# Kernel optimization log

Measured on AMD Instinct MI355X. Metric: run time of the kernel, lower is better.

## Reference

```python
import jax, jax.numpy as jnp
import numpy as np
from jax import lax

B, T, V, E, H = 32, 512, 32000, 300, 256
TRANSITION = 0.1
TEMP = 0.01
BUDGET_PCT = 30.0
NEG = -1e9


def setup_inputs() -> dict:
    key = jax.random.key(0)
    ks = jax.random.split(key, 10)
    sc = lambda k, shape, s=0.05: (jax.random.normal(k, shape, jnp.float32) * s)
    x = jax.random.randint(ks[0], (B, T), 0, V)
    mask = jnp.ones((B, T), bool)
    embed = sc(ks[1], (V, E), 0.1)
    w_ih_f = sc(ks[2], (E, 4 * H))
    w_hh_f = sc(ks[3], (H, 4 * H))
    b_f = jnp.zeros((4 * H,), jnp.float32)
    w_ih_b = sc(ks[4], (E, 4 * H))
    w_hh_b = sc(ks[5], (H, 4 * H))
    b_b = jnp.zeros((4 * H,), jnp.float32)
    w_out = sc(ks[6], (2 * H, 1), 0.1)
    b_out = jnp.zeros((1,), jnp.float32)
    return {"x": x, "current_epoch": 0, "mask": mask, "embed": embed,
            "w_ih_f": w_ih_f, "w_hh_f": w_hh_f, "b_f": b_f,
            "w_ih_b": w_ih_b, "w_hh_b": w_hh_b, "b_b": b_b,
            "w_out": w_out, "b_out": b_out}


def _lstm_dir(emb, mask, Wi, Wh, b):
    # masked LSTM equivalent to pack_padded_sequence; gate order i,f,g,o (torch)
    bs, tl, _ = emb.shape
    h0 = jnp.zeros((bs, Wh.shape[0]), emb.dtype)
    xg = emb @ Wi + b  # [B,T,4H]

    def step(carry, inp):
        h, c = carry
        xg_t, m_t = inp
        g = xg_t + h @ Wh
        i, f, gg, o = jnp.split(g, 4, axis=-1)
        i = jax.nn.sigmoid(i); f = jax.nn.sigmoid(f)
        gg = jnp.tanh(gg); o = jax.nn.sigmoid(o)
        c_new = f * c + i * gg
        h_new = o * jnp.tanh(c_new)
        m = m_t[:, None]
        h_new = jnp.where(m, h_new, h)
        c_new = jnp.where(m, c_new, c)
        return (h_new, c_new), jnp.where(m, h_new, 0.0)

    _, hs = lax.scan(step, (h0, h0), (xg.transpose(1, 0, 2), mask.T))
    return hs.transpose(1, 0, 2)


def _forward(x, mask, embed, w_ih_f, w_hh_f, b_f, w_ih_b, w_hh_b, b_b, w_out, b_out):
    emb = embed[x]  # [B,T,E] (dropout disabled / eval)
    h_f = _lstm_dir(emb, mask, w_ih_f, w_hh_f, b_f)
    h_b = jnp.flip(_lstm_dir(jnp.flip(emb, 1), jnp.flip(mask, 1), w_ih_b, w_hh_b, b_b), 1)
    h = jnp.concatenate([h_f, h_b], axis=-1)  # [B,T,2H]
    scores = (h @ w_out + b_out)[..., 0]  # [B,T]

    lengths = mask.sum(1)
    pos = jnp.arange(T)
    # unary for state 0 (selected); padded positions forced off
    u0 = jnp.where(pos[None, :] < lengths[:, None], scores / TEMP, NEG)
    # transition[t,0,0] = transition/temp for t <= length, else 0;  t in 0..T
    tvals = jnp.where(jnp.arange(T + 1)[None, :] <= lengths[:, None], TRANSITION / TEMP, 0.0)
    budget = jnp.round(BUDGET_PCT / 100.0 * lengths)
    Cmax = int(round(BUDGET_PCT / 100.0 * T)) + 1  # static count dim

    def logZ(u0_):
        alpha = jnp.full((u0_.shape[0], Cmax, 2), NEG, u0_.dtype)
        alpha = alpha.at[:, 1, 0].set(u0_[:, 0] + tvals[:, 0])  # start in state0 (count 1)
        alpha = alpha.at[:, 0, 1].set(0.0)                       # start in state1 (count 0)

        def step(a, inp):
            u0_t, t_t = inp
            a_shift = jnp.concatenate([jnp.full((a.shape[0], 1, 2), NEG, a.dtype), a[:, :-1, :]], axis=1)
            m0 = jnp.logaddexp(a_shift[..., 0] + t_t[:, None], a_shift[..., 1])
            m1 = jnp.logaddexp(a[..., 0], a[..., 1])
            return jnp.stack([u0_t[:, None] + m0, m1], axis=-1), None

        alpha, _ = lax.scan(step, alpha, (u0_[:, 1:].T, tvals[:, 1:T].T))
        final = jnp.stack([alpha[..., 0] + tvals[:, T][:, None], alpha[..., 1]], axis=-1)
        allowed = (jnp.arange(Cmax)[None, :] <= budget[:, None])[..., None]
        lz = jax.nn.logsumexp(jnp.where(allowed, final, NEG).reshape(final.shape[0], -1), axis=-1)
        return lz.sum()

    # marginal p(z_i=1) = d logZ / d u0_i  (budget-constrained chain marginals)
    z = jax.grad(logZ)(u0)
    return jnp.where(mask, z, 0.0)


def reference(x, current_epoch, mask, embed, w_ih_f, w_hh_f, b_f, w_ih_b, w_hh_b, b_b, w_out, b_out):
    return _forward(x, mask, embed, w_ih_f, w_hh_f, b_f, w_ih_b, w_hh_b, b_b, w_out, b_out)
```

## Files before the change

kernel.cpp:

```cpp
#include <hip/hip_runtime.h>
#include <math.h>

#define BB 32
#define TT_LEN 512
#define EE 300
#define HH 256
#define G4 1024
#define CMAX 155
#define TRANS_T 10.0f
#define NEGF -1.0e9f
#define INV_TEMP 100.0f
#define AST_STRIDE 159

#define NCH_L2 8
#define NREG 24

typedef _Float16 half2v __attribute__((ext_vector_type(2)));
typedef _Float16 half8 __attribute__((ext_vector_type(8)));
typedef float f32x4 __attribute__((ext_vector_type(4)));

__device__ __forceinline__ float la(float x, float y) {
  float m = fmaxf(x, y);
  float d = fminf(x, y) - m;
  return m + __logf(1.0f + __expf(d));
}

__device__ __forceinline__ float sigm(float x) {
  return 1.0f / (1.0f + __expf(-x));
}

__device__ __forceinline__ float dot2acc(unsigned int wd, unsigned int hd, float acc) {
#if __has_builtin(__builtin_amdgcn_fdot2)
  return __builtin_amdgcn_fdot2(__builtin_bit_cast(half2v, wd),
                                __builtin_bit_cast(half2v, hd), acc, false);
#else
  half2v a = __builtin_bit_cast(half2v, wd);
  half2v b = __builtin_bit_cast(half2v, hd);
  return acc + (float)a.x * (float)b.x + (float)a.y * (float)b.y;
#endif
}

__device__ __forceinline__ unsigned int packh(float a, float b) {
  half2v hp;
  hp.x = (_Float16)a;
  hp.y = (_Float16)b;
  return __builtin_bit_cast(unsigned int, hp);
}

__global__ void prep_weights(const float* wi_f, const float* wi_b,
                             const float* wh_f, const float* wh_b,
                             const float* b_f, const float* b_b,
                             unsigned int* wi_frag, float* b_p,
                             unsigned int* wlds_h, unsigned int* wstr_h) {
  int idx = blockIdx.x * blockDim.x + threadIdx.x;
  int stride = gridDim.x * blockDim.x;
  for (int i = idx; i < 2 * 64 * 10 * 64 * 4; i += stride) {
    int u4 = i >> 2, d = i & 3;
    int lane = u4 & 63;
    int kk = (u4 >> 6) % 10;
    int nb = (u4 / 640) & 63;
    int dir = u4 / (640 * 64);
    int l15 = lane & 15, quad = lane >> 4;
    int n = nb * 16 + l15;
    int g = n & 3, u = n >> 2;
    int k0 = kk * 32 + quad * 8 + 2 * d;
    const float* src = dir ? wi_b : wi_f;
    float v0 = (k0 < EE) ? src[(size_t)k0 * G4 + g * HH + u] : 0.0f;
    float v1 = (k0 + 1 < EE) ? src[(size_t)(k0 + 1) * G4 + g * HH + u] : 0.0f;
    wi_frag[i] = packh(v0, v1);
  }
  for (int i = idx; i < 2 * NCH_L2 * 4096; i += stride) {
    int dir = i / (NCH_L2 * 4096);
    int r = i % (NCH_L2 * 4096);
    int c = r / 4096;
    int r2 = r % 4096;
    int j = r2 >> 2, d = r2 & 3;
    int g = j & 3, u = j >> 2;
    int k0 = 8 * c + 2 * d;
    const float* src = dir ? wh_b : wh_f;
    wlds_h[i] = packh(src[k0 * G4 + g * HH + u], src[(k0 + 1) * G4 + g * HH + u]);
  }
  for (int i = idx; i < 2 * NREG * 4096; i += stride) {
    int dir = i / (NREG * 4096);
    int r = i % (NREG * 4096);
    int gch = r / 4096;
    int r2 = r % 4096;
    int j = r2 >> 2, d = r2 & 3;
    int g = j & 3, u = j >> 2;
    int k0 = 64 + 8 * gch + 2 * d;
    const float* src = dir ? wh_b : wh_f;
    wstr_h[i] = packh(src[k0 * G4 + g * HH + u], src[(k0 + 1) * G4 + g * HH + u]);
  }
  for (int i = idx; i < 2 * G4; i += stride) {
    int dir = i / G4;
    int j = i % G4;
    int g = j & 3, u = j >> 2;
    const float* src = dir ? b_b : b_f;
    b_p[i] = src[g * HH + u];
  }
}

__global__ void gather_emb(const int* x, const float* embed, uint4* emb_frag) {
  int mblk = blockIdx.x;
  int t = threadIdx.x;
  __shared__ int xs[16];
  if (t < 16) xs[t] = x[mblk * 16 + t];
  __syncthreads();
  for (int slot = t; slot < 640; slot += 256) {
    int kk = slot >> 6;
    int lane = slot & 63;
    int l15 = lane & 15, quad = lane >> 4;
    int row = xs[l15];
    int kbase = kk * 32 + quad * 8;
    const float* src = embed + (size_t)row * EE;
    float v[8];
#pragma unroll
    for (int e = 0; e < 8; ++e) v[e] = (kbase + e < EE) ? src[kbase + e] : 0.0f;
    uint4 o;
    o.x = packh(v[0], v[1]);
    o.y = packh(v[2], v[3]);
    o.z = packh(v[4], v[5]);
    o.w = packh(v[6], v[7]);
    emb_frag[(size_t)(mblk * 10 + kk) * 64 + lane] = o;
  }
}

__global__ __launch_bounds__(256) void xg_mfma(
    const uint4* __restrict__ emb_frag, const uint4* __restrict__ wi_frag,
    const float* __restrict__ b_p, float* __restrict__ xg) {
  int dir = blockIdx.z;
  int w = threadIdx.x >> 6;
  int lane = threadIdx.x & 63;
  int l15 = lane & 15, quad = lane >> 4;
  int mblk = blockIdx.y * 4 + w;

  const uint4* abase = emb_frag + (size_t)mblk * 10 * 64 + lane;
  f32x4 acc[4];
#pragma unroll
  for (int nt = 0; nt < 4; ++nt) acc[nt] = (f32x4){0.f, 0.f, 0.f, 0.f};

#pragma unroll
  for (int kk = 0; kk < 10; ++kk) {
    half8 a = __builtin_bit_cast(half8, abase[kk * 64]);
#pragma unroll
    for (int nt = 0; nt < 4; ++nt) {
      int nb = blockIdx.x * 4 + nt;
      half8 b = __builtin_bit_cast(
          half8, wi_frag[((size_t)(dir * 64 + nb) * 10 + kk) * 64 + lane]);
      acc[nt] = __builtin_amdgcn_mfma_f32_16x16x32_f16(a, b, acc[nt], 0, 0, 0);
    }
  }
#pragma unroll
  for (int nt = 0; nt < 4; ++nt) {
    int n = (blockIdx.x * 4 + nt) * 16 + l15;
    float bias = b_p[dir * G4 + n];
#pragma unroll
    for (int r = 0; r < 4; ++r) {
      int m = mblk * 16 + quad * 4 + r;
      xg[((size_t)dir * (BB * TT_LEN) + m) * G4 + n] = acc[nt][r] + bias;
    }
  }
}

__global__ __launch_bounds__(512, 2) void lstm_ck(
    const float* __restrict__ xg, const unsigned int* __restrict__ wlds_h,
    const uint4* __restrict__ wstr, const float* __restrict__ w_out,
    float* __restrict__ scores_part) {
  int bid = blockIdx.x;
  int dir = bid >> 5, b = bid & 31;
  int t = threadIdx.x;
  int lane = t & 63, wid = t >> 6;

  __shared__ uint4 wlds[NCH_L2 * 1024];
  __shared__ uint4 hpk4[32];
  __shared__ float gates[1024];
  __shared__ float wpart[2][4];

  const uint4* wsrcl = (const uint4*)wlds_h + (size_t)dir * (NCH_L2 * 1024);
  for (int i = t; i < NCH_L2 * 1024; i += 512) wlds[i] = wsrcl[i];
  const uint4* wsb = wstr + (size_t)dir * (NREG * 1024);
  uint4 wr0[NREG], wr1[NREG];
#pragma unroll
  for (int g = 0; g < NREG; ++g) {
    wr0[g] = wsb[g * 1024 + t];
    wr1[g] = wsb[g * 1024 + t + 512];
  }
  if (t < 32) hpk4[t] = uint4{0, 0, 0, 0};
  __syncthreads();

  const float* xgbase =
      xg + (size_t)(dir * (BB * TT_LEN) + b * TT_LEN) * G4 + t;
  float wo = (t < HH) ? w_out[dir * HH + t] : 0.0f;
  float cstate = 0.0f;

  int t0 = dir ? (TT_LEN - 1) : 0;
  float xgn0 = xgbase[(size_t)t0 * G4];
  float xgn1 = xgbase[(size_t)t0 * G4 + 512];

#pragma unroll 1
  for (int s = 0; s < TT_LEN; ++s) {
    int tt = dir ? (TT_LEN - 1 - s) : s;
    float acc0a = xgn0, acc1a = xgn1;
    float acc0b = 0.0f, acc1b = 0.0f;
    if (s + 1 < TT_LEN) {
      int t2 = dir ? (TT_LEN - 2 - s) : (s + 1);
      xgn0 = xgbase[(size_t)t2 * G4];
      xgn1 = xgbase[(size_t)t2 * G4 + 512];
    }
#pragma unroll
    for (int c = 0; c < NCH_L2; ++c) {
      uint4 h = hpk4[c];
      uint4 w0 = wlds[c * 1024 + t];
      uint4 w1 = wlds[c * 1024 + 512 + t];
      acc0a = dot2acc(w0.x, h.x, acc0a);
      acc0a = dot2acc(w0.y, h.y, acc0a);
      acc0a = dot2acc(w0.z, h.z, acc0a);
      acc0a = dot2acc(w0.w, h.w, acc0a);
      acc1a = dot2acc(w1.x, h.x, acc1a);
      acc1a = dot2acc(w1.y, h.y, acc1a);
      acc1a = dot2acc(w1.z, h.z, acc1a);
      acc1a = dot2acc(w1.w, h.w, acc1a);
    }
#pragma unroll
    for (int g = 0; g < NREG; ++g) {
      uint4 h = hpk4[NCH_L2 + g];
      if (g < 12) {
        acc0a = dot2acc(wr0[g].x, h.x, acc0a);
        acc0a = dot2acc(wr0[g].y, h.y, acc0a);
        acc0a = dot2acc(wr0[g].z, h.z, acc0a);
        acc0a = dot2acc(wr0[g].w, h.w, acc0a);
        acc1a = dot2acc(wr1[g].x, h.x, acc1a);
        acc1a = dot2acc(wr1[g].y, h.y, acc1a);
        acc1a = dot2acc(wr1[g].z, h.z, acc1a);
        acc1a = dot2acc(wr1[g].w, h.w, acc1a);
      } else {
        acc0b = dot2acc(wr0[g].x, h.x, acc0b);
        acc0b = dot2acc(wr0[g].y, h.y, acc0b);
        acc0b = dot2acc(wr0[g].z, h.z, acc0b);
        acc0b = dot2acc(wr0[g].w, h.w, acc0b);
        acc1b = dot2acc(wr1[g].x, h.x, acc1b);
        acc1b = dot2acc(wr1[g].y, h.y, acc1b);
        acc1b = dot2acc(wr1[g].z, h.z, acc1b);
        acc1b = dot2acc(wr1[g].w, h.w, acc1b);
      }
    }
    gates[t] = acc0a + acc0b;
    gates[512 + t] = acc1a + acc1b;
    __syncthreads();

    if (t < HH) {
      float4 g4 = ((const float4*)gates)[t];
      float ig = sigm(g4.x);
      float fg = sigm(g4.y);
      float gg = tanhf(g4.z);
      float og = sigm(g4.w);
      cstate = fg * cstate + ig * gg;
      float h = og * tanhf(cstate);
      float prod = h * wo;
#pragma unroll
      for (int off = 32; off > 0; off >>= 1) prod += __shfl_down(prod, off, 64);
      if (lane == 0) wpart[s & 1][wid] = prod;
      float hn = __shfl_down(h, 1, 64);
      if (!(t & 1)) ((unsigned int*)hpk4)[t >> 1] = packh(h, hn);
    }
    __syncthreads();
    if (t == 0) {
      scores_part[(size_t)(dir * BB + b) * TT_LEN + tt] =
          wpart[s & 1][0] + wpart[s & 1][1] + wpart[s & 1][2] + wpart[s & 1][3];
    }
  }
}

__global__ __launch_bounds__(128) void dp3(const float* __restrict__ scores_part,
                                           const float* __restrict__ b_out,
                                           float* __restrict__ ast_g,
                                           float* __restrict__ bst_g,
                                           float* __restrict__ lzv) {
  int b = blockIdx.x;
  int l = threadIdx.x & 63;
  int w = threadIdx.x >> 6;
  const float* spf = scores_part + (size_t)b * TT_LEN;
  const float* spb = scores_part + (size_t)(BB + b) * TT_LEN;
  float bo = b_out[0];

  float ur[8];
#pragma unroll
  for (int i = 0; i < 8; ++i)
    ur[i] = (spf[i * 64 + l] + spb[i * 64 + l] + bo) * INV_TEMP;

  if (w == 0) {
    float* ast = ast_g + (size_t)b * TT_LEN * AST_STRIDE;
    int lm1 = (l + 63) & 63;
    float a0[3], a1[3];
    float u00 = __shfl(ur[0], 0, 64);
    a0[0] = (l == 1) ? (u00 + TRANS_T) : NEGF;
    a0[1] = NEGF;
    a0[2] = NEGF;
    a1[0] = (l == 0) ? 0.0f : NEGF;
    a1[1] = NEGF;
    a1[2] = NEGF;
    ast[l] = a0[0];
    ast[64 + l] = a0[1];
    if (l < 27) ast[128 + l] = a0[2];

#pragma unroll
    for (int ch = 0; ch < 8; ++ch) {
      float uc = ur[ch];
#pragma unroll 4
      for (int tt = (ch == 0 ? 1 : 0); tt < 64; ++tt) {
        int t = ch * 64 + tt;
        float u0t = __shfl(uc, tt, 64);
        float w0a = __shfl(a0[0], lm1, 64);
        float w1a = __shfl(a0[1], lm1, 64);
        float w2a = __shfl(a0[2], lm1, 64);
        float w0b = __shfl(a1[0], lm1, 64);
        float w1b = __shfl(a1[1], lm1, 64);
        float w2b = __shfl(a1[2], lm1, 64);
        float p0a = (l == 0) ? NEGF : w0a;
        float p1a = (l == 0) ? w0a : w1a;
        float p2a = (l == 0) ? w1a : w2a;
        float p0b = (l == 0) ? NEGF : w0b;
        float p1b = (l == 0) ? w0b : w1b;
        float p2b = (l == 0) ? w1b : w2b;
        float n00 = u0t + la(p0a + TRANS_T, p0b);
        float n01 = u0t + la(p1a + TRANS_T, p1b);
        float n02 = u0t + la(p2a + TRANS_T, p2b);
        float n10 = la(a0[0], a1[0]);
        float n11 = la(a0[1], a1[1]);
        float n12 = la(a0[2], a1[2]);
        a0[0] = n00;
        a0[1] = n01;
        a0[2] = (l < 27) ? n02 : NEGF;
        a1[0] = n10;
        a1[1] = n11;
        a1[2] = (l < 27) ? n12 : NEGF;
        float* astr = ast + (size_t)t * AST_STRIDE;
        astr[l] = a0[0];
        astr[64 + l] = a0[1];
        if (l < 27) astr[128 + l] = a0[2];
      }
    }
    float f00 = a0[0] + TRANS_T, f01 = a0[1] + TRANS_T, f02 = a0[2] + TRANS_T;
    float m = fmaxf(fmaxf(fmaxf(f00, f01), fmaxf(f02, a1[0])),
                    fmaxf(a1[1], a1[2]));
#pragma unroll
    for (int off = 32; off > 0; off >>= 1) m = fmaxf(m, __shfl_xor(m, off, 64));
    float es = __expf(f00 - m) + __expf(f01 - m) + __expf(f02 - m) +
               __expf(a1[0] - m) + __expf(a1[1] - m) + __expf(a1[2] - m);
#pragma unroll
    for (int off = 32; off > 0; off >>= 1) es += __shfl_xor(es, off, 64);
    if (l == 0) lzv[b] = m + __logf(es);
  } else {
    float* bst = bst_g + (size_t)b * TT_LEN * AST_STRIDE;
    int lp1 = (l + 1) & 63;
    float b0[3], b1[3];
    b0[0] = TRANS_T;
    b0[1] = TRANS_T;
    b0[2] = (l < 27) ? TRANS_T : NEGF;
    b1[0] = 0.0f;
    b1[1] = 0.0f;
    b1[2] = (l < 27) ? 0.0f : NEGF;
    {
      float* br = bst + (size_t)(TT_LEN - 1) * AST_STRIDE;
      br[l] = b0[0];
      br[64 + l] = b0[1];
      if (l < 27) br[128 + l] = b0[2];
    }
#pragma unroll
    for (int ch = 7; ch >= 0; --ch) {
      float uc = ur[ch];
#pragma unroll 4
      for (int tt = 63; tt >= (ch == 0 ? 1 : 0); --tt) {
        int t = ch * 64 + tt;
        float u0t = __shfl(uc, tt, 64);
        float w0 = __shfl(b0[0], lp1, 64);
        float w1 = __shfl(b0[1], lp1, 64);
        float w2 = __shfl(b0[2], lp1, 64);
        float x2 = (l == 63) ? NEGF : w2;
        float x1 = (l == 63) ? w2 : w1;
        float x0 = (l == 63) ? w1 : w0;
        float nb00 = la(u0t + TRANS_T + x0, b1[0]);
        float nb01 = la(u0t + TRANS_T + x1, b1[1]);
        float nb02 = la(u0t + TRANS_T + x2, b1[2]);
        float nb10 = la(u0t + x0, b1[0]);
        float nb11 = la(u0t + x1, b1[1]);
        float nb12 = la(u0t + x2, b1[2]);
        b0[0] = nb00;
        b0[1] = nb01;
        b0[2] = (l < 27) ? nb02 : NEGF;
        b1[0] = nb10;
        b1[1] = nb11;
        b1[2] = (l < 27) ? nb12 : NEGF;
        float* br = bst + (size_t)(t - 1) * AST_STRIDE;
        br[l] = b0[0];
        br[64 + l] = b0[1];
        if (l < 27) br[128 + l] = b0[2];
      }
    }
  }
}

__global__ __launch_bounds__(256) void marg(const float* __restrict__ ast_g,
                                            const float* __restrict__ bst_g,
                                            const float* __restrict__ lzv,
                                            float* __restrict__ out) {
  int row = blockIdx.x * 4 + (threadIdx.x >> 6);
  int l = threadIdx.x & 63;
  int b = row >> 9;
  const float* ar = ast_g + (size_t)row * AST_STRIDE;
  const float* br = bst_g + (size_t)row * AST_STRIDE;
  float lz = lzv[b];
  float s = __expf(ar[l] + br[l] - lz) + __expf(ar[64 + l] + br[64 + l] - lz) +
            ((l < 27) ? __expf(ar[128 + l] + br[128 + l] - lz) : 0.0f);
#pragma unroll
  for (int off = 32; off > 0; off >>= 1) s += __shfl_xor(s, off, 64);
  if (l == 0) out[row] = s;
}

extern "C" void kernel_launch(void* const* d_in, const int* in_sizes, int n_in,
                              void* d_out, int out_size, void* d_ws, size_t ws_size,
                              hipStream_t stream) {
  const int* x = (const int*)d_in[0];
  const float* embed = (const float*)d_in[3];
  const float* wi_f = (const float*)d_in[4];
  const float* wh_f = (const float*)d_in[5];
  const float* bf = (const float*)d_in[6];
  const float* wi_b = (const float*)d_in[7];
  const float* wh_b = (const float*)d_in[8];
  const float* bbias = (const float*)d_in[9];
  const float* w_out = (const float*)d_in[10];
  const float* b_out = (const float*)d_in[11];

  float* ws = (float*)d_ws;
  float* b_p = ws;
  unsigned int* wlds_h = (unsigned int*)(b_p + 2 * G4);
  unsigned int* wstr_h = wlds_h + 2 * NCH_L2 * 4096;
  unsigned int* wi_frag = wstr_h + 2 * NREG * 4096;
  uint4* emb_frag = (uint4*)(wi_frag + 2 * 64 * 10 * 64 * 4);
  float* bst_g = (float*)emb_frag;
  float* xg = (float*)(emb_frag + (size_t)1024 * 10 * 64);
  float* scores_part = xg + (size_t)2 * BB * TT_LEN * G4;
  float* lzv = scores_part + 2 * BB * TT_LEN;
  float* ast_g = lzv + 64;
  float* outp = (float*)d_out;

  prep_weights<<<256, 256, 0, stream>>>(wi_f, wi_b, wh_f, wh_b, bf, bbias,
                                        wi_frag, b_p, wlds_h, wstr_h);
  gather_emb<<<(BB * TT_LEN) / 16, 256, 0, stream>>>(x, embed, emb_frag);
  dim3 g1(16, 256, 2);
  xg_mfma<<<g1, 256, 0, stream>>>(emb_frag, (const uint4*)wi_frag, b_p, xg);
  lstm_ck<<<64, 512, 0, stream>>>(xg, wlds_h, (const uint4*)wstr_h, w_out,
                                  scores_part);
  dp3<<<BB, 128, 0, stream>>>(scores_part, b_out, ast_g, bst_g, lzv);
  marg<<<(BB * TT_LEN) / 4, 256, 0, stream>>>(ast_g, bst_g, lzv, outp);
}
```

Baseline: 1.553 ms.

## Batch LSTM recurrence over 16 sequences per block using MFMA

Replaces the per-sequence dot2 LSTM recurrence (64 blocks, one batch row each) with an MFMA-based recurrence where each block handles 16 batch rows of one direction. The recurrent weights are split between registers and LDS, h is kept in swizzled LDS as fp16, and xg is stored in fp16 fragment layout to halve traffic. The score projection moves to a separate kernel that reads a stored fp16 h tensor. This cuts the per-step matvec cost with matrix cores, but only 4 blocks run, and it adds fp16 rounding of xg and h plus an extra global round trip for h.

```diff
diff --git a/kernel.cpp b/kernel.cpp
--- a/kernel.cpp
+++ b/kernel.cpp
@@ -12,9 +12,6 @@
 #define INV_TEMP 100.0f
 #define AST_STRIDE 159
 
-#define NCH_L2 8
-#define NREG 24
-
 typedef _Float16 half2v __attribute__((ext_vector_type(2)));
 typedef _Float16 half8 __attribute__((ext_vector_type(8)));
 typedef float f32x4 __attribute__((ext_vector_type(4)));
@@ -29,15 +26,10 @@
   return 1.0f / (1.0f + __expf(-x));
 }
 
-__device__ __forceinline__ float dot2acc(unsigned int wd, unsigned int hd, float acc) {
-#if __has_builtin(__builtin_amdgcn_fdot2)
-  return __builtin_amdgcn_fdot2(__builtin_bit_cast(half2v, wd),
-                                __builtin_bit_cast(half2v, hd), acc, false);
-#else
-  half2v a = __builtin_bit_cast(half2v, wd);
-  half2v b = __builtin_bit_cast(half2v, hd);
-  return acc + (float)a.x * (float)b.x + (float)a.y * (float)b.y;
-#endif
+__device__ __forceinline__ float tanh_f(float x) {
+  x = fminf(fmaxf(x, -15.f), 15.f);
+  float e = __expf(2.f * x);
+  return (e - 1.f) * __frcp_rn(e + 1.f);
 }
 
 __device__ __forceinline__ unsigned int packh(float a, float b) {
@@ -47,11 +39,27 @@
   return __builtin_bit_cast(unsigned int, hp);
 }
 
+__device__ __forceinline__ float2 h2f(unsigned int d) {
+  half2v h = __builtin_bit_cast(half2v, d);
+  return make_float2((float)h.x, (float)h.y);
+}
+
+__device__ __forceinline__ unsigned short f16b(float x) {
+  _Float16 h = (_Float16)x;
+  return __builtin_bit_cast(unsigned short, h);
+}
+
+__device__ __forceinline__ int nmap_col(int n) {
+  int g = (n >> 4) & 3;
+  int u = (n >> 7) * 32 + ((n >> 6) & 1) * 16 + (n & 15);
+  return g * HH + u;
+}
+
 __global__ void prep_weights(const float* wi_f, const float* wi_b,
                              const float* wh_f, const float* wh_b,
                              const float* b_f, const float* b_b,
                              unsigned int* wi_frag, float* b_p,
-                             unsigned int* wlds_h, unsigned int* wstr_h) {
+                             uint4* whr, uint4* whl) {
   int idx = blockIdx.x * blockDim.x + threadIdx.x;
   int stride = gridDim.x * blockDim.x;
   for (int i = idx; i < 2 * 64 * 10 * 64 * 4; i += stride) {
@@ -61,50 +69,46 @@
     int nb = (u4 / 640) & 63;
     int dir = u4 / (640 * 64);
     int l15 = lane & 15, quad = lane >> 4;
-    int n = nb * 16 + l15;
-    int g = n & 3, u = n >> 2;
+    int col = nmap_col(nb * 16 + l15);
     int k0 = kk * 32 + quad * 8 + 2 * d;
     const float* src = dir ? wi_b : wi_f;
-    float v0 = (k0 < EE) ? src[(size_t)k0 * G4 + g * HH + u] : 0.0f;
-    float v1 = (k0 + 1 < EE) ? src[(size_t)(k0 + 1) * G4 + g * HH + u] : 0.0f;
+    float v0 = (k0 < EE) ? src[(size_t)k0 * G4 + col] : 0.0f;
+    float v1 = (k0 + 1 < EE) ? src[(size_t)(k0 + 1) * G4 + col] : 0.0f;
     wi_frag[i] = packh(v0, v1);
   }
-  for (int i = idx; i < 2 * NCH_L2 * 4096; i += stride) {
-    int dir = i / (NCH_L2 * 4096);
-    int r = i % (NCH_L2 * 4096);
-    int c = r / 4096;
-    int r2 = r % 4096;
-    int j = r2 >> 2, d = r2 & 3;
-    int g = j & 3, u = j >> 2;
-    int k0 = 8 * c + 2 * d;
+  for (int i = idx; i < 2 * 8 * 64 * 64; i += stride) {
+    int lane = i & 63;
+    int nb = (i >> 6) & 63;
+    int kt = (i >> 12) & 7;
+    int dir = i >> 15;
+    int c = lane & 15, q = lane >> 4;
+    int col = nmap_col(nb * 16 + c);
+    int k0 = kt * 32 + q * 8;
     const float* src = dir ? wh_b : wh_f;
-    wlds_h[i] = packh(src[k0 * G4 + g * HH + u], src[(k0 + 1) * G4 + g * HH + u]);
-  }
-  for (int i = idx; i < 2 * NREG * 4096; i += stride) {
-    int dir = i / (NREG * 4096);
-    int r = i % (NREG * 4096);
-    int gch = r / 4096;
-    int r2 = r % 4096;
-    int j = r2 >> 2, d = r2 & 3;
-    int g = j & 3, u = j >> 2;
-    int k0 = 64 + 8 * gch + 2 * d;
-    const float* src = dir ? wh_b : wh_f;
-    wstr_h[i] = packh(src[k0 * G4 + g * HH + u], src[(k0 + 1) * G4 + g * HH + u]);
+    uint4 o;
+    o.x = packh(src[(size_t)(k0 + 0) * G4 + col], src[(size_t)(k0 + 1) * G4 + col]);
+    o.y = packh(src[(size_t)(k0 + 2) * G4 + col], src[(size_t)(k0 + 3) * G4 + col]);
+    o.z = packh(src[(size_t)(k0 + 4) * G4 + col], src[(size_t)(k0 + 5) * G4 + col]);
+    o.w = packh(src[(size_t)(k0 + 6) * G4 + col], src[(size_t)(k0 + 7) * G4 + col]);
+    if (kt < 6)
+      whr[((size_t)(dir * 6 + kt) * 64 + nb) * 64 + lane] = o;
+    else
+      whl[((size_t)(dir * 2 + kt - 6) * 64 + nb) * 64 + lane] = o;
   }
   for (int i = idx; i < 2 * G4; i += stride) {
     int dir = i / G4;
     int j = i % G4;
-    int g = j & 3, u = j >> 2;
     const float* src = dir ? b_b : b_f;
-    b_p[i] = src[g * HH + u];
+    b_p[i] = src[nmap_col(j)];
   }
 }
 
 __global__ void gather_emb(const int* x, const float* embed, uint4* emb_frag) {
   int mblk = blockIdx.x;
   int t = threadIdx.x;
+  int bg = mblk >> 9, tloc = mblk & 511;
   __shared__ int xs[16];
-  if (t < 16) xs[t] = x[mblk * 16 + t];
+  if (t < 16) xs[t] = x[(bg * 16 + t) * TT_LEN + tloc];
   __syncthreads();
   for (int slot = t; slot < 640; slot += 256) {
     int kk = slot >> 6;
@@ -127,11 +131,11 @@
 
 __global__ __launch_bounds__(256) void xg_mfma(
     const uint4* __restrict__ emb_frag, const uint4* __restrict__ wi_frag,
-    const float* __restrict__ b_p, float* __restrict__ xg) {
+    const float* __restrict__ b_p, uint4* __restrict__ xg_frag) {
   int dir = blockIdx.z;
   int w = threadIdx.x >> 6;
   int lane = threadIdx.x & 63;
-  int l15 = lane & 15, quad = lane >> 4;
+  int l15 = lane & 15;
   int mblk = blockIdx.y * 4 + w;
 
   const uint4* abase = emb_frag + (size_t)mblk * 10 * 64 + lane;
@@ -151,124 +155,140 @@
     }
   }
 #pragma unroll
-  for (int nt = 0; nt < 4; ++nt) {
-    int n = (blockIdx.x * 4 + nt) * 16 + l15;
-    float bias = b_p[dir * G4 + n];
-#pragma unroll
-    for (int r = 0; r < 4; ++r) {
-      int m = mblk * 16 + quad * 4 + r;
-      xg[((size_t)dir * (BB * TT_LEN) + m) * G4 + n] = acc[nt][r] + bias;
-    }
-  }
-}
-
-__global__ __launch_bounds__(512, 2) void lstm_ck(
-    const float* __restrict__ xg, const unsigned int* __restrict__ wlds_h,
-    const uint4* __restrict__ wstr, const float* __restrict__ w_out,
-    float* __restrict__ scores_part) {
-  int bid = blockIdx.x;
-  int dir = bid >> 5, b = bid & 31;
+  for (int ntp = 0; ntp < 2; ++ntp) {
+    float bA = b_p[dir * G4 + (blockIdx.x * 4 + 2 * ntp) * 16 + l15];
+    float bB = b_p[dir * G4 + (blockIdx.x * 4 + 2 * ntp + 1) * 16 + l15];
+    f32x4 aA = acc[2 * ntp], aB = acc[2 * ntp + 1];
+    uint4 o;
+    o.x = packh(aA[0] + bA, aA[1] + bA);
+    o.y = packh(aA[2] + bA, aA[3] + bA);
+    o.z = packh(aB[0] + bB, aB[1] + bB);
+    o.w = packh(aB[2] + bB, aB[3] + bB);
+    xg_frag[((size_t)(dir * 1024 + mblk) * 32 + blockIdx.x * 2 + ntp) * 64 + lane] = o;
+  }
+}
+
+__global__ __launch_bounds__(512, 2) void lstm_mfma(
+    const uint4* __restrict__ xg_frag, const uint4* __restrict__ whr,
+    const uint4* __restrict__ whl, unsigned short* __restrict__ h16g) {
+  int dir = blockIdx.x >> 1, bg = blockIdx.x & 1;
   int t = threadIdx.x;
-  int lane = t & 63, wid = t >> 6;
-
-  __shared__ uint4 wlds[NCH_L2 * 1024];
-  __shared__ uint4 hpk4[32];
-  __shared__ float gates[1024];
-  __shared__ float wpart[2][4];
-
-  const uint4* wsrcl = (const uint4*)wlds_h + (size_t)dir * (NCH_L2 * 1024);
-  for (int i = t; i < NCH_L2 * 1024; i += 512) wlds[i] = wsrcl[i];
-  const uint4* wsb = wstr + (size_t)dir * (NREG * 1024);
-  uint4 wr0[NREG], wr1[NREG];
-#pragma unroll
-  for (int g = 0; g < NREG; ++g) {
-    wr0[g] = wsb[g * 1024 + t];
-    wr1[g] = wsb[g * 1024 + t + 512];
-  }
-  if (t < 32) hpk4[t] = uint4{0, 0, 0, 0};
+  int lane = t & 63, w = t >> 6;
+  int c = lane & 15, q = lane >> 4;
+
+  __shared__ uint4 wlds[2 * 64 * 64];
+  __shared__ uint4 wlds5[16 * 64];
+  __shared__ unsigned short hsw[16 * 256];
+
+  for (int i = t; i < 8192; i += 512) wlds[i] = whl[(size_t)dir * 8192 + i];
+  for (int i = t; i < 1024; i += 512) {
+    int widx = i >> 7, sub = (i >> 6) & 1, l2 = i & 63;
+    wlds5[i] = whr[((size_t)(dir * 6 + 5) * 64 + widx * 8 + 6 + sub) * 64 + l2];
+  }
+  for (int i = t; i < 2048; i += 512) ((unsigned int*)hsw)[i] = 0;
+
+  uint4 wreg[46];
+#pragma unroll
+  for (int kt = 0; kt < 5; ++kt)
+#pragma unroll
+    for (int nt = 0; nt < 8; ++nt)
+      wreg[kt * 8 + nt] =
+          whr[((size_t)(dir * 6 + kt) * 64 + w * 8 + nt) * 64 + lane];
+#pragma unroll
+  for (int nt = 0; nt < 6; ++nt)
+    wreg[40 + nt] = whr[((size_t)(dir * 6 + 5) * 64 + w * 8 + nt) * 64 + lane];
+
+  float cst[8];
+#pragma unroll
+  for (int i = 0; i < 8; ++i) cst[i] = 0.f;
+
+  const uint4* xgb =
+      xg_frag + ((size_t)(dir * 1024 + bg * 512) * 32 + w * 4) * 64 + lane;
+  unsigned short* hgb = h16g + (size_t)dir * 4194304 + bg * 16 + 4 * q;
+  const int xk = (c & 7) << 3;
+
   __syncthreads();
-
-  const float* xgbase =
-      xg + (size_t)(dir * (BB * TT_LEN) + b * TT_LEN) * G4 + t;
-  float wo = (t < HH) ? w_out[dir * HH + t] : 0.0f;
-  float cstate = 0.0f;
-
-  int t0 = dir ? (TT_LEN - 1) : 0;
-  float xgn0 = xgbase[(size_t)t0 * G4];
-  float xgn1 = xgbase[(size_t)t0 * G4 + 512];
 
 #pragma unroll 1
   for (int s = 0; s < TT_LEN; ++s) {
     int tt = dir ? (TT_LEN - 1 - s) : s;
-    float acc0a = xgn0, acc1a = xgn1;
-    float acc0b = 0.0f, acc1b = 0.0f;
-    if (s + 1 < TT_LEN) {
-      int t2 = dir ? (TT_LEN - 2 - s) : (s + 1);
-      xgn0 = xgbase[(size_t)t2 * G4];
-      xgn1 = xgbase[(size_t)t2 * G4 + 512];
-    }
-#pragma unroll
-    for (int c = 0; c < NCH_L2; ++c) {
-      uint4 h = hpk4[c];
-      uint4 w0 = wlds[c * 1024 + t];
-      uint4 w1 = wlds[c * 1024 + 512 + t];
-      acc0a = dot2acc(w0.x, h.x, acc0a);
-      acc0a = dot2acc(w0.y, h.y, acc0a);
-      acc0a = dot2acc(w0.z, h.z, acc0a);
-      acc0a = dot2acc(w0.w, h.w, acc0a);
-      acc1a = dot2acc(w1.x, h.x, acc1a);
-      acc1a = dot2acc(w1.y, h.y, acc1a);
-      acc1a = dot2acc(w1.z, h.z, acc1a);
-      acc1a = dot2acc(w1.w, h.w, acc1a);
-    }
-#pragma unroll
-    for (int g = 0; g < NREG; ++g) {
-      uint4 h = hpk4[NCH_L2 + g];
-      if (g < 12) {
-        acc0a = dot2acc(wr0[g].x, h.x, acc0a);
-        acc0a = dot2acc(wr0[g].y, h.y, acc0a);
-        acc0a = dot2acc(wr0[g].z, h.z, acc0a);
-        acc0a = dot2acc(wr0[g].w, h.w, acc0a);
-        acc1a = dot2acc(wr1[g].x, h.x, acc1a);
-        acc1a = dot2acc(wr1[g].y, h.y, acc1a);
-        acc1a = dot2acc(wr1[g].z, h.z, acc1a);
-        acc1a = dot2acc(wr1[g].w, h.w, acc1a);
-      } else {
-        acc0b = dot2acc(wr0[g].x, h.x, acc0b);
-        acc0b = dot2acc(wr0[g].y, h.y, acc0b);
-        acc0b = dot2acc(wr0[g].z, h.z, acc0b);
-        acc0b = dot2acc(wr0[g].w, h.w, acc0b);
-        acc1b = dot2acc(wr1[g].x, h.x, acc1b);
-        acc1b = dot2acc(wr1[g].y, h.y, acc1b);
-        acc1b = dot2acc(wr1[g].z, h.z, acc1b);
-        acc1b = dot2acc(wr1[g].w, h.w, acc1b);
+    const uint4* xp = xgb + (size_t)tt * 2048;
+    uint4 xa = xp[0];
+    uint4 xb = xp[64];
+    uint4 xc, xd;
+    f32x4 D[8];
+#pragma unroll
+    for (int nt = 0; nt < 8; ++nt) D[nt] = (f32x4){0.f, 0.f, 0.f, 0.f};
+#pragma unroll
+    for (int kt = 0; kt < 8; ++kt) {
+      if (kt == 2) { xc = xp[128]; xd = xp[192]; }
+      half8 A = *(const half8*)(hsw + (c * 256 + ((kt * 32 + q * 8) ^ xk)));
+#pragma unroll
+      for (int nt = 0; nt < 8; ++nt) {
+        uint4 bw;
+        if (kt < 5)
+          bw = wreg[kt * 8 + nt];
+        else if (kt == 5)
+          bw = (nt < 6) ? wreg[40 + nt] : wlds5[(w * 2 + nt - 6) * 64 + lane];
+        else
+          bw = wlds[((kt - 6) * 64 + w * 8 + nt) * 64 + lane];
+        D[nt] = __builtin_amdgcn_mfma_f32_16x16x32_f16(
+            A, __builtin_bit_cast(half8, bw), D[nt], 0, 0, 0);
       }
     }
-    gates[t] = acc0a + acc0b;
-    gates[512 + t] = acc1a + acc1b;
     __syncthreads();
-
-    if (t < HH) {
-      float4 g4 = ((const float4*)gates)[t];
-      float ig = sigm(g4.x);
-      float fg = sigm(g4.y);
-      float gg = tanhf(g4.z);
-      float og = sigm(g4.w);
-      cstate = fg * cstate + ig * gg;
-      float h = og * tanhf(cstate);
-      float prod = h * wo;
-#pragma unroll
-      for (int off = 32; off > 0; off >>= 1) prod += __shfl_down(prod, off, 64);
-      if (lane == 0) wpart[s & 1][wid] = prod;
-      float hn = __shfl_down(h, 1, 64);
-      if (!(t & 1)) ((unsigned int*)hpk4)[t >> 1] = packh(h, hn);
+#pragma unroll
+    for (int ph = 0; ph < 2; ++ph) {
+      uint4 va = ph ? xc : xa;
+      uint4 vb = ph ? xd : xb;
+      float2 p0 = h2f(va.x), p1 = h2f(va.y), p2 = h2f(va.z), p3 = h2f(va.w);
+      float2 p4 = h2f(vb.x), p5 = h2f(vb.y), p6 = h2f(vb.z), p7 = h2f(vb.w);
+      float xi[4] = {p0.x, p0.y, p1.x, p1.y};
+      float xf[4] = {p2.x, p2.y, p3.x, p3.y};
+      float xgv[4] = {p4.x, p4.y, p5.x, p5.y};
+      float xo[4] = {p6.x, p6.y, p7.x, p7.y};
+      int u = w * 32 + ph * 16 + c;
+      float hv[4];
+#pragma unroll
+      for (int r = 0; r < 4; ++r) {
+        float I = sigm(D[ph * 4 + 0][r] + xi[r]);
+        float F = sigm(D[ph * 4 + 1][r] + xf[r]);
+        float G = tanh_f(D[ph * 4 + 2][r] + xgv[r]);
+        float O = sigm(D[ph * 4 + 3][r] + xo[r]);
+        float cn = F * cst[ph * 4 + r] + I * G;
+        cst[ph * 4 + r] = cn;
+        float h = O * tanh_f(cn);
+        hv[r] = h;
+        int m = 4 * q + r;
+        hsw[m * 256 + (u ^ ((m & 7) << 3))] = f16b(h);
+      }
+      uint2 pk;
+      pk.x = packh(hv[0], hv[1]);
+      pk.y = packh(hv[2], hv[3]);
+      *(uint2*)(hgb + ((size_t)tt * 8192 + u * 32)) = pk;
     }
     __syncthreads();
-    if (t == 0) {
-      scores_part[(size_t)(dir * BB + b) * TT_LEN + tt] =
-          wpart[s & 1][0] + wpart[s & 1][1] + wpart[s & 1][2] + wpart[s & 1][3];
-    }
-  }
+  }
+}
+
+__global__ __launch_bounds__(64) void hscore(
+    const unsigned short* __restrict__ h16g, const float* __restrict__ w_out,
+    float* __restrict__ scores_part) {
+  int dt = blockIdx.x;
+  int dir = dt >> 9, tpos = dt & 511;
+  int l = threadIdx.x;
+  int b = l & 31, uh = l >> 5;
+  const unsigned short* base =
+      h16g + (((size_t)dir * 512 + tpos) * 256 + uh * 128) * 32 + b;
+  const float* wo = w_out + dir * HH + uh * 128;
+  float s = 0.f;
+#pragma unroll 8
+  for (int u = 0; u < 128; ++u) {
+    _Float16 hv = __builtin_bit_cast(_Float16, base[(size_t)u * 32]);
+    s += (float)hv * wo[u];
+  }
+  s += __shfl_down(s, 32, 64);
+  if (uh == 0) scores_part[((size_t)dir * BB + b) * TT_LEN + tpos] = s;
 }
 
 __global__ __launch_bounds__(128) void dp3(const float* __restrict__ scores_part,
@@ -433,24 +453,25 @@
 
   float* ws = (float*)d_ws;
   float* b_p = ws;
-  unsigned int* wlds_h = (unsigned int*)(b_p + 2 * G4);
-  unsigned int* wstr_h = wlds_h + 2 * NCH_L2 * 4096;
-  unsigned int* wi_frag = wstr_h + 2 * NREG * 4096;
-  uint4* emb_frag = (uint4*)(wi_frag + 2 * 64 * 10 * 64 * 4);
-  float* bst_g = (float*)emb_frag;
-  float* xg = (float*)(emb_frag + (size_t)1024 * 10 * 64);
-  float* scores_part = xg + (size_t)2 * BB * TT_LEN * G4;
+  unsigned int* wi_frag = (unsigned int*)(b_p + 2 * G4);
+  uint4* whr = (uint4*)(wi_frag + 2 * 64 * 10 * 64 * 4);
+  uint4* whl = whr + 49152;
+  uint4* emb_frag = whl + 16384;
+  uint4* xg_frag = emb_frag + 655360;
+  unsigned short* h16g = (unsigned short*)(xg_frag + 4194304);
+  float* scores_part = (float*)(h16g + 8388608);
   float* lzv = scores_part + 2 * BB * TT_LEN;
   float* ast_g = lzv + 64;
+  float* bst_g = (float*)emb_frag;
   float* outp = (float*)d_out;
 
   prep_weights<<<256, 256, 0, stream>>>(wi_f, wi_b, wh_f, wh_b, bf, bbias,
-                                        wi_frag, b_p, wlds_h, wstr_h);
+                                        wi_frag, b_p, whr, whl);
   gather_emb<<<(BB * TT_LEN) / 16, 256, 0, stream>>>(x, embed, emb_frag);
   dim3 g1(16, 256, 2);
-  xg_mfma<<<g1, 256, 0, stream>>>(emb_frag, (const uint4*)wi_frag, b_p, xg);
-  lstm_ck<<<64, 512, 0, stream>>>(xg, wlds_h, (const uint4*)wstr_h, w_out,
-                                  scores_part);
+  xg_mfma<<<g1, 256, 0, stream>>>(emb_frag, (const uint4*)wi_frag, b_p, xg_frag);
+  lstm_mfma<<<4, 512, 0, stream>>>(xg_frag, whr, whl, h16g);
+  hscore<<<2 * TT_LEN, 64, 0, stream>>>(h16g, w_out, scores_part);
   dp3<<<BB, 128, 0, stream>>>(scores_part, b_out, ast_g, bst_g, lzv);
   marg<<<(BB * TT_LEN) / 4, 256, 0, stream>>>(ast_g, bst_g, lzv, outp);
 }
```

After: 3.108 ms. +100.1%, slower.
